# Kernel tuning notes

Measured on AMD Instinct MI355X. Metric: run time of the kernel, lower is better.

Reference implementation:

```python
import jax, jax.numpy as jnp
import numpy as np

SEQ_LEN = 1024
WINDOW = 32
NUM_HEADS = 16
BATCH = 8
DIM = 1024


def make_local_mask(seq_len=SEQ_LEN, window=WINDOW):
    # True = position is MASKED (disallowed), matching the torch bool attn_mask.
    # torch allows j in [i - window//2, i + window//2] inclusive.
    i = np.arange(seq_len)[:, None]
    j = np.arange(seq_len)[None, :]
    half = window // 2
    allowed = (j >= i - half) & (j <= i + half)
    return jnp.asarray(~allowed)


def setup_inputs() -> dict:
    key = jax.random.key(0)
    k_x, k_wi, k_wo = jax.random.split(key, 3)
    scale_in = 1.0 / np.sqrt(DIM)
    return {
        "x": jax.random.normal(k_x, (BATCH, SEQ_LEN, DIM), dtype=jnp.float32),
        "w_in": jax.random.normal(k_wi, (3 * DIM, DIM), dtype=jnp.float32) * scale_in,
        "b_in": jnp.zeros((3 * DIM,), dtype=jnp.float32),
        "w_out": jax.random.normal(k_wo, (DIM, DIM), dtype=jnp.float32) * scale_in,
        "b_out": jnp.zeros((DIM,), dtype=jnp.float32),
        "mask": make_local_mask(),
    }


def reference(x, w_in, b_in, w_out, b_out, mask):
    B, S, D = x.shape
    H = NUM_HEADS
    hd = D // H
    # fused in-projection (torch nn.MultiheadAttention self-attn path)
    qkv = x @ w_in.T + b_in                      # [B, S, 3D]
    q, k, v = jnp.split(qkv, 3, axis=-1)
    q = q.reshape(B, S, H, hd).transpose(0, 2, 1, 3)  # [B, H, S, hd]
    k = k.reshape(B, S, H, hd).transpose(0, 2, 1, 3)
    v = v.reshape(B, S, H, hd).transpose(0, 2, 1, 3)
    scores = jnp.einsum("bhqd,bhkd->bhqk", q, k) / jnp.sqrt(jnp.asarray(hd, x.dtype))
    neg = jnp.asarray(jnp.finfo(x.dtype).min, x.dtype)
    scores = jnp.where(mask[None, None, :, :], neg, scores)
    attn = jax.nn.softmax(scores, axis=-1)
    ctx = jnp.einsum("bhqk,bhkd->bhqd", attn, v)  # [B, H, S, hd]
    ctx = ctx.transpose(0, 2, 1, 3).reshape(B, S, D)
    return ctx @ w_out.T + b_out
```

## Files before the change

### kernel.cpp

```cpp
#include <hip/hip_runtime.h>

#define S_LEN   1024
#define NH      16
#define HD      64
#define BATCHN  8
#define DMODEL  1024
#define HALF_W  16

typedef __attribute__((ext_vector_type(8))) short bf16x8;
typedef __attribute__((ext_vector_type(4))) float f32x4;

__device__ __forceinline__ unsigned short f2bf(float f) {
  unsigned u = __builtin_bit_cast(unsigned, f);
  u += 0x7fffu + ((u >> 16) & 1u);
  return (unsigned short)(u >> 16);
}
__device__ __forceinline__ float bf2f(unsigned short h) {
  return __builtin_bit_cast(float, ((unsigned)h) << 16);
}

__device__ __forceinline__ void gload_lds16(const void* g, void* l) {
  __builtin_amdgcn_global_load_lds(
      (const __attribute__((address_space(1))) void*)g,
      (__attribute__((address_space(3))) void*)l, 16, 0, 0);
}

__global__ __launch_bounds__(256) void cvt_bf16_kernel(
    const float* __restrict__ in, unsigned short* __restrict__ out, int n4) {
  int t = blockIdx.x * 256 + threadIdx.x;
  if (t >= n4) return;
  float4 v = reinterpret_cast<const float4*>(in)[t];
  ushort4 o = make_ushort4(f2bf(v.x), f2bf(v.y), f2bf(v.z), f2bf(v.w));
  reinterpret_cast<ushort4*>(out)[t] = o;
}

#define MFMA_BF16 __builtin_amdgcn_mfma_f32_16x16x32_bf16

__global__ __launch_bounds__(512, 2) void gemm_inproj_kernel(
    const unsigned short* __restrict__ A,
    const unsigned short* __restrict__ B,
    const float* __restrict__ bias,
    unsigned short* __restrict__ C) {
  __shared__ __align__(16) unsigned short lds[81920];

  const int tid  = threadIdx.x;
  const int lane = tid & 63;
  const int wid  = tid >> 6;
  const int wm   = wid >> 2;
  const int wn   = wid & 3;
  const int lgrp = lane >> 4;
  const int l15  = lane & 15;

  const int sid = (blockIdx.x & 7) * 32 + (blockIdx.x >> 3);
  const int tileM = (sid >> 3) * 256;
  const int tileN = (sid & 7) * 384;

  const int srow = tid >> 2;
  const int scol = ((tid & 3) ^ ((tid >> 3) & 3)) * 8;
  const unsigned short* gA_s = A + (size_t)(tileM + srow) * 1024 + scol;
  const unsigned short* gB_s = B + (size_t)(tileN + srow) * 1024 + scol;

  const int fch  = (lgrp ^ ((l15 >> 1) & 3)) * 8;
  const int arow = (wm * 128 + l15) * 32 + fch;
  const int brow = (wn * 96 + l15) * 32 + fch;

  f32x4 acc[48] = {};

#define STG(S) do { const int _q = (S) & 3;                                \
    const unsigned short* _ga = gA_s + (S) * 32;                           \
    const unsigned short* _gb = gB_s + (S) * 32;                           \
    gload_lds16(_ga,          &lds[_q * 8192 + tid * 8]);                  \
    gload_lds16(_ga + 131072, &lds[_q * 8192 + 4096 + tid * 8]);           \
    gload_lds16(_gb,          &lds[32768 + _q * 12288 + tid * 8]);         \
    gload_lds16(_gb + 131072, &lds[32768 + _q * 12288 + 4096 + tid * 8]);  \
    gload_lds16(_gb + 262144, &lds[32768 + _q * 12288 + 8192 + tid * 8]);  \
  } while (0)

#define M24(MB)                                                            \
    acc[(MB+0)*6+0] = MFMA_BF16(a0_, b0_, acc[(MB+0)*6+0], 0, 0, 0);       \
    acc[(MB+0)*6+1] = MFMA_BF16(a0_, b1_, acc[(MB+0)*6+1], 0, 0, 0);       \
    acc[(MB+0)*6+2] = MFMA_BF16(a0_, b2_, acc[(MB+0)*6+2], 0, 0, 0);       \
    acc[(MB+0)*6+3] = MFMA_BF16(a0_, b3_, acc[(MB+0)*6+3], 0, 0, 0);       \
    acc[(MB+0)*6+4] = MFMA_BF16(a0_, b4_, acc[(MB+0)*6+4], 0, 0, 0);       \
    acc[(MB+0)*6+5] = MFMA_BF16(a0_, b5_, acc[(MB+0)*6+5], 0, 0, 0);       \
    acc[(MB+1)*6+0] = MFMA_BF16(a1_, b0_, acc[(MB+1)*6+0], 0, 0, 0);       \
    acc[(MB+1)*6+1] = MFMA_BF16(a1_, b1_, acc[(MB+1)*6+1], 0, 0, 0);       \
    acc[(MB+1)*6+2] = MFMA_BF16(a1_, b2_, acc[(MB+1)*6+2], 0, 0, 0);       \
    acc[(MB+1)*6+3] = MFMA_BF16(a1_, b3_, acc[(MB+1)*6+3], 0, 0, 0);       \
    acc[(MB+1)*6+4] = MFMA_BF16(a1_, b4_, acc[(MB+1)*6+4], 0, 0, 0);       \
    acc[(MB+1)*6+5] = MFMA_BF16(a1_, b5_, acc[(MB+1)*6+5], 0, 0, 0);       \
    acc[(MB+2)*6+0] = MFMA_BF16(a2_, b0_, acc[(MB+2)*6+0], 0, 0, 0);       \
    acc[(MB+2)*6+1] = MFMA_BF16(a2_, b1_, acc[(MB+2)*6+1], 0, 0, 0);       \
    acc[(MB+2)*6+2] = MFMA_BF16(a2_, b2_, acc[(MB+2)*6+2], 0, 0, 0);       \
    acc[(MB+2)*6+3] = MFMA_BF16(a2_, b3_, acc[(MB+2)*6+3], 0, 0, 0);       \
    acc[(MB+2)*6+4] = MFMA_BF16(a2_, b4_, acc[(MB+2)*6+4], 0, 0, 0);       \
    acc[(MB+2)*6+5] = MFMA_BF16(a2_, b5_, acc[(MB+2)*6+5], 0, 0, 0);       \
    acc[(MB+3)*6+0] = MFMA_BF16(a3_, b0_, acc[(MB+3)*6+0], 0, 0, 0);       \
    acc[(MB+3)*6+1] = MFMA_BF16(a3_, b1_, acc[(MB+3)*6+1], 0, 0, 0);       \
    acc[(MB+3)*6+2] = MFMA_BF16(a3_, b2_, acc[(MB+3)*6+2], 0, 0, 0);       \
    acc[(MB+3)*6+3] = MFMA_BF16(a3_, b3_, acc[(MB+3)*6+3], 0, 0, 0);       \
    acc[(MB+3)*6+4] = MFMA_BF16(a3_, b4_, acc[(MB+3)*6+4], 0, 0, 0);       \
    acc[(MB+3)*6+5] = MFMA_BF16(a3_, b5_, acc[(MB+3)*6+5], 0, 0, 0);

  STG(0); STG(1); STG(2);

#pragma unroll 1
  for (int p = 0; p < 32; ++p) {
    if (p < 30)       { asm volatile("s_waitcnt vmcnt(10)" ::: "memory"); }
    else if (p == 30) { asm volatile("s_waitcnt vmcnt(5)"  ::: "memory"); }
    else              { asm volatile("s_waitcnt vmcnt(0)"  ::: "memory"); }
    __builtin_amdgcn_sched_barrier(0);
    __builtin_amdgcn_s_barrier();

    if (p <= 28) STG(p + 3);

    const int slot = p & 3;
    const unsigned short* pa = &lds[slot * 8192 + arow];
    const unsigned short* pb = &lds[32768 + slot * 12288 + brow];

    bf16x8 b0_ = *(const bf16x8*)(pb);
    bf16x8 b1_ = *(const bf16x8*)(pb + 512);
    bf16x8 b2_ = *(const bf16x8*)(pb + 1024);
    bf16x8 b3_ = *(const bf16x8*)(pb + 1536);
    bf16x8 b4_ = *(const bf16x8*)(pb + 2048);
    bf16x8 b5_ = *(const bf16x8*)(pb + 2560);
    bf16x8 a0_ = *(const bf16x8*)(pa);
    bf16x8 a1_ = *(const bf16x8*)(pa + 512);
    bf16x8 a2_ = *(const bf16x8*)(pa + 1024);
    bf16x8 a3_ = *(const bf16x8*)(pa + 1536);
    asm volatile("s_waitcnt lgkmcnt(0)" ::: "memory");
    __builtin_amdgcn_sched_barrier(0);
    __builtin_amdgcn_s_setprio(1);
    M24(0)
    __builtin_amdgcn_s_setprio(0);

    a0_ = *(const bf16x8*)(pa + 2048);
    a1_ = *(const bf16x8*)(pa + 2560);
    a2_ = *(const bf16x8*)(pa + 3072);
    a3_ = *(const bf16x8*)(pa + 3584);
    asm volatile("s_waitcnt lgkmcnt(0)" ::: "memory");
    __builtin_amdgcn_sched_barrier(0);
    __builtin_amdgcn_s_setprio(1);
    M24(4)
    __builtin_amdgcn_s_setprio(0);
  }
#undef STG
#undef M24

#pragma unroll
  for (int nt = 0; nt < 6; ++nt) {
    const int col = tileN + wn * 96 + nt * 16 + l15;
    const float bs = bias[col];
#pragma unroll
    for (int mt = 0; mt < 8; ++mt) {
      const int row0 = tileM + wm * 128 + mt * 16 + lgrp * 4;
#pragma unroll
      for (int rr = 0; rr < 4; ++rr)
        C[(size_t)(row0 + rr) * 3072 + col] = f2bf(acc[mt * 6 + nt][rr] + bs);
    }
  }
}

__global__ __launch_bounds__(512, 2) void gemm_outproj_kernel(
    const unsigned short* __restrict__ A,
    const unsigned short* __restrict__ B,
    const float* __restrict__ bias,
    float* __restrict__ Cv) {
  __shared__ __align__(16) unsigned short sA[2][2][4096];
  __shared__ __align__(16) unsigned short sB[2][2][8192];

  const int tid  = threadIdx.x;
  const int lane = tid & 63;
  const int wid  = tid >> 6;
  const int wm   = wid >> 2;
  const int wn   = wid & 3;
  const int lgrp = lane >> 4;
  const int l15  = lane & 15;

  const int sid = (blockIdx.x & 7) * 32 + (blockIdx.x >> 3);
  const int tileM = (sid >> 2) * 128;
  const int tileN = (sid & 3) * 256;

  const int srow = tid >> 2;
  const int scol = ((tid & 3) ^ ((tid >> 3) & 3)) * 8;
  const unsigned short* gA_s = A + (size_t)(tileM + srow) * 1024 + scol;
  const unsigned short* gB_s = B + (size_t)(tileN + srow) * 1024 + scol;

  const int fch  = (lgrp ^ ((l15 >> 1) & 3)) * 8;
  const int arow = (wm * 64 + l15) * 32 + fch;
  const int brow = (wn * 64 + l15) * 32 + fch;

  f32x4 acc[4][4] = {};

#define SSA(KT, BUF, KH) do {                                              \
    gload_lds16(gA_s + (KT) * 64 + (KH) * 32, &sA[BUF][KH][wid * 512]);    \
  } while (0)
#define SSB(KT, BUF, KH) do {                                              \
    const unsigned short* _sb = gB_s + (KT) * 64 + (KH) * 32;              \
    gload_lds16(_sb,          &sB[BUF][KH][wid * 512]);                    \
    gload_lds16(_sb + 131072, &sB[BUF][KH][4096 + wid * 512]);             \
  } while (0)

#define GATE(NSTR) do {                                                    \
    asm volatile("s_waitcnt vmcnt(" NSTR ")" ::: "memory");                \
    __builtin_amdgcn_sched_barrier(0);                                     \
    __builtin_amdgcn_s_barrier(); } while (0)

#define PH1(BUF, KH, STGA, STGB) do {                                      \
    STGA; STGB;                                                            \
    const unsigned short* _pa = &sA[BUF][KH][arow];                        \
    const unsigned short* _pb = &sB[BUF][KH][brow];                        \
    bf16x8 a0_ = *(const bf16x8*)(_pa);                                    \
    bf16x8 a1_ = *(const bf16x8*)(_pa + 512);                              \
    bf16x8 a2_ = *(const bf16x8*)(_pa + 1024);                             \
    bf16x8 a3_ = *(const bf16x8*)(_pa + 1536);                             \
    bf16x8 nb0 = *(const bf16x8*)(_pb);                                    \
    bf16x8 nb1 = *(const bf16x8*)(_pb + 512);                              \
    bf16x8 nb2 = *(const bf16x8*)(_pb + 1024);                             \
    bf16x8 nb3 = *(const bf16x8*)(_pb + 1536);                             \
    asm volatile("s_waitcnt lgkmcnt(0)" ::: "memory");                     \
    __builtin_amdgcn_sched_barrier(0);                                     \
    __builtin_amdgcn_s_setprio(1);                                         \
    acc[0][0] = MFMA_BF16(a0_, nb0, acc[0][0], 0, 0, 0);                   \
    acc[0][1] = MFMA_BF16(a0_, nb1, acc[0][1], 0, 0, 0);                   \
    acc[0][2] = MFMA_BF16(a0_, nb2, acc[0][2], 0, 0, 0);                   \
    acc[0][3] = MFMA_BF16(a0_, nb3, acc[0][3], 0, 0, 0);                   \
    acc[1][0] = MFMA_BF16(a1_, nb0, acc[1][0], 0, 0, 0);                   \
    acc[1][1] = MFMA_BF16(a1_, nb1, acc[1][1], 0, 0, 0);                   \
    acc[1][2] = MFMA_BF16(a1_, nb2, acc[1][2], 0, 0, 0);                   \
    acc[1][3] = MFMA_BF16(a1_, nb3, acc[1][3], 0, 0, 0);                   \
    acc[2][0] = MFMA_BF16(a2_, nb0, acc[2][0], 0, 0, 0);                   \
    acc[2][1] = MFMA_BF16(a2_, nb1, acc[2][1], 0, 0, 0);                   \
    acc[2][2] = MFMA_BF16(a2_, nb2, acc[2][2], 0, 0, 0);                   \
    acc[2][3] = MFMA_BF16(a2_, nb3, acc[2][3], 0, 0, 0);                   \
    acc[3][0] = MFMA_BF16(a3_, nb0, acc[3][0], 0, 0, 0);                   \
    acc[3][1] = MFMA_BF16(a3_, nb1, acc[3][1], 0, 0, 0);                   \
    acc[3][2] = MFMA_BF16(a3_, nb2, acc[3][2], 0, 0, 0);                   \
    acc[3][3] = MFMA_BF16(a3_, nb3, acc[3][3], 0, 0, 0);                   \
    __builtin_amdgcn_s_setprio(0);                                         \
  } while (0)
#define NOSTG ((void)0)

  SSA(0, 0, 0); SSB(0, 0, 0);
  SSA(0, 0, 1); SSB(0, 0, 1);
  SSA(1, 1, 0); SSB(1, 1, 0);

#pragma unroll 1
  for (int kt = 0; kt < 14; kt += 2) {
    GATE("6"); PH1(0, 0, SSA(kt + 1, 1, 1), SSB(kt + 1, 1, 1));
    GATE("6"); PH1(0, 1, SSA(kt + 2, 0, 0), SSB(kt + 2, 0, 0));
    GATE("6"); PH1(1, 0, SSA(kt + 2, 0, 1), SSB(kt + 2, 0, 1));
    GATE("6"); PH1(1, 1, SSA(kt + 3, 1, 0), SSB(kt + 3, 1, 0));
  }
  GATE("6"); PH1(0, 0, SSA(15, 1, 1), SSB(15, 1, 1));
  GATE("6"); PH1(0, 1, NOSTG, NOSTG);
  GATE("3"); PH1(1, 0, NOSTG, NOSTG);
  GATE("0"); PH1(1, 1, NOSTG, NOSTG);

#undef SSA
#undef SSB
#undef GATE
#undef PH1
#undef NOSTG

#pragma unroll
  for (int nt = 0; nt < 4; ++nt) {
    const int col = tileN + wn * 64 + nt * 16 + l15;
    const float bs = bias[col];
#pragma unroll
    for (int mt = 0; mt < 4; ++mt) {
      const int row0 = tileM + wm * 64 + mt * 16 + lgrp * 4;
#pragma unroll
      for (int rr = 0; rr < 4; ++rr)
        Cv[(size_t)(row0 + rr) * 1024 + col] = acc[mt][nt][rr] + bs;
    }
  }
}

#define KST 72
#define PST 104

__global__ __launch_bounds__(256) void attn_local_kernel(
    const unsigned short* __restrict__ qkv, unsigned short* __restrict__ ctx) {
  __shared__ __align__(16) unsigned short sKP[96 * KST];
  __shared__ __align__(16) unsigned short sQ[64 * KST];
  __shared__ __align__(16) unsigned short sVT[64 * PST];

  const int tid  = threadIdx.x;
  const int lane = tid & 63;
  const int wid  = tid >> 6;
  const int qc   = lane & 15;
  const int lgrp = lane >> 4;

  const int qb = blockIdx.x & 15;
  const int h  = (blockIdx.x >> 4) & 15;
  const int b  = blockIdx.x >> 8;
  const int i0 = qb * 64;

  const unsigned short* hb = qkv + (size_t)b * S_LEN * 3072 + (size_t)h * HD;

#pragma unroll
  for (int it = 0; it < 3; ++it) {
    int c  = it * 256 + tid;
    int r  = c >> 3;
    int d0 = (c & 7) * 8;
    int j  = i0 - 16 + r;
    bf16x8 kv = {}, vv = {};
    if (0 <= j && j < S_LEN) {
      const unsigned short* rp = hb + (size_t)j * 3072;
      kv = *reinterpret_cast<const bf16x8*>(rp + DMODEL + d0);
      vv = *reinterpret_cast<const bf16x8*>(rp + 2 * DMODEL + d0);
    }
    *reinterpret_cast<bf16x8*>(&sKP[r * KST + d0]) = kv;
#pragma unroll
    for (int jj = 0; jj < 8; ++jj) {
      int dd = (jj + c) & 7;
      sVT[(d0 + dd) * PST + r] = (unsigned short)vv[dd];
    }
  }
#pragma unroll
  for (int it = 0; it < 2; ++it) {
    int c  = it * 256 + tid;
    int r  = c >> 3;
    int d0 = (c & 7) * 8;
    bf16x8 qv = *reinterpret_cast<const bf16x8*>(hb + (size_t)(i0 + r) * 3072 + d0);
    *reinterpret_cast<bf16x8*>(&sQ[r * KST + d0]) = qv;
  }
  __syncthreads();

  const int q0 = wid * 16;

  bf16x8 bq[2];
#pragma unroll
  for (int ks = 0; ks < 2; ++ks)
    bq[ks] = *reinterpret_cast<const bf16x8*>(
        &sQ[(q0 + qc) * KST + ks * 32 + lgrp * 8]);

  f32x4 st[6] = {};
#pragma unroll
  for (int kt = 0; kt < 6; ++kt) {
#pragma unroll
    for (int ks = 0; ks < 2; ++ks) {
      bf16x8 fa = *reinterpret_cast<const bf16x8*>(
          &sKP[(kt * 16 + qc) * KST + ks * 32 + lgrp * 8]);
      st[kt] = __builtin_amdgcn_mfma_f32_16x16x32_bf16(fa, bq[ks], st[kt], 0, 0, 0);
    }
  }
  __syncthreads();

  const int q = q0 + qc;
  float pv[6][4];
  float mx = -3.0e38f;
#pragma unroll
  for (int kt = 0; kt < 6; ++kt)
#pragma unroll
    for (int rr = 0; rr < 4; ++rr) {
      int kk = kt * 16 + lgrp * 4 + rr;
      int j  = i0 - 16 + kk;
      bool ok = (j >= 0) && (j < S_LEN) && (kk >= q) && (kk <= q + 32);
      float s = ok ? st[kt][rr] * 0.125f : -3.0e38f;
      pv[kt][rr] = s;
      mx = fmaxf(mx, s);
    }
  mx = fmaxf(mx, __shfl_xor(mx, 16, 64));
  mx = fmaxf(mx, __shfl_xor(mx, 32, 64));

  float rsum = 0.f;
#pragma unroll
  for (int kt = 0; kt < 6; ++kt)
#pragma unroll
    for (int rr = 0; rr < 4; ++rr) {
      float p = __expf(pv[kt][rr] - mx);
      pv[kt][rr] = p;
      rsum += p;
    }
  rsum += __shfl_xor(rsum, 16, 64);
  rsum += __shfl_xor(rsum, 32, 64);
  const float inv = 1.0f / rsum;

  unsigned short* sP = sKP;
#pragma unroll
  for (int kt = 0; kt < 6; ++kt) {
    ushort4 w = make_ushort4(f2bf(pv[kt][0]), f2bf(pv[kt][1]),
                             f2bf(pv[kt][2]), f2bf(pv[kt][3]));
    *reinterpret_cast<ushort4*>(&sP[(q0 + qc) * PST + kt * 16 + lgrp * 4]) = w;
  }

  bf16x8 pb[3];
#pragma unroll
  for (int ks = 0; ks < 3; ++ks)
    pb[ks] = *reinterpret_cast<const bf16x8*>(
        &sP[(q0 + qc) * PST + ks * 32 + lgrp * 8]);

  f32x4 ct[4] = {};
#pragma unroll
  for (int dt = 0; dt < 4; ++dt)
#pragma unroll
    for (int ks = 0; ks < 3; ++ks) {
      bf16x8 fa = *reinterpret_cast<const bf16x8*>(
          &sVT[(dt * 16 + qc) * PST + ks * 32 + lgrp * 8]);
      ct[dt] = __builtin_amdgcn_mfma_f32_16x16x32_bf16(fa, pb[ks], ct[dt], 0, 0, 0);
    }

  unsigned short* op =
      ctx + ((size_t)b * S_LEN + i0 + q0 + qc) * DMODEL + h * HD;
#pragma unroll
  for (int dt = 0; dt < 4; ++dt) {
    ushort4 w = make_ushort4(
        f2bf(ct[dt][0] * inv), f2bf(ct[dt][1] * inv),
        f2bf(ct[dt][2] * inv), f2bf(ct[dt][3] * inv));
    *reinterpret_cast<ushort4*>(op + dt * 16 + lgrp * 4) = w;
  }
}

extern "C" void kernel_launch(void* const* d_in, const int* in_sizes, int n_in,
                              void* d_out, int out_size, void* d_ws, size_t ws_size,
                              hipStream_t stream) {
  const float* x     = (const float*)d_in[0];
  const float* w_in  = (const float*)d_in[1];
  const float* b_in  = (const float*)d_in[2];
  const float* w_out = (const float*)d_in[3];
  const float* b_out = (const float*)d_in[4];
  float* out = (float*)d_out;

  unsigned short* xb   = (unsigned short*)d_ws;
  unsigned short* wib  = xb  + (size_t)8192 * 1024;
  unsigned short* wob  = wib + (size_t)3072 * 1024;
  unsigned short* qkv  = wob + (size_t)1024 * 1024;
  unsigned short* ctxb = qkv + (size_t)8192 * 3072;

  cvt_bf16_kernel<<<8192, 256, 0, stream>>>(x, xb, (8192 * 1024) / 4);
  cvt_bf16_kernel<<<3072, 256, 0, stream>>>(w_in, wib, (3072 * 1024) / 4);
  cvt_bf16_kernel<<<1024, 256, 0, stream>>>(w_out, wob, (1024 * 1024) / 4);

  gemm_inproj_kernel<<<256, 512, 0, stream>>>(xb, wib, b_in, qkv);

  attn_local_kernel<<<BATCHN * NH * (S_LEN / 64), 256, 0, stream>>>(qkv, ctxb);

  gemm_outproj_kernel<<<256, 512, 0, stream>>>(ctxb, wob, b_out, out);
}
```

Baseline: 121.2 us.

## Double-buffer LDS fragment registers to prefetch next k-step during MFMAs

Restructures the in-projection GEMM main loop into a ping-pong register scheme. The A/B fragments for the next k-slice are read from LDS while the current slice's MFMAs run, with partial lgkmcnt waits in place of full drains. The vmcnt waits are tightened to match the earlier fragment reads. This is meant to hide LDS read latency behind matrix work, at the cost of many more live VGPRs (about 24 extra bf16x8 registers) with occupancy fixed at 2 blocks of 512 threads, so spilling is a risk.

```diff
diff --git a/kernel.cpp b/kernel.cpp
--- a/kernel.cpp
+++ b/kernel.cpp
@@ -65,6 +65,12 @@
   const int brow = (wn * 96 + l15) * 32 + fch;
 
   f32x4 acc[48] = {};
+
+  bf16x8 b0A = {}, b1A = {}, b2A = {}, b3A = {}, b4A = {}, b5A = {};
+  bf16x8 a0A = {}, a1A = {}, a2A = {}, a3A = {};
+  bf16x8 b0B = {}, b1B = {}, b2B = {}, b3B = {}, b4B = {}, b5B = {};
+  bf16x8 a0B = {}, a1B = {}, a2B = {}, a3B = {};
+  bf16x8 sa0 = {}, sa1 = {}, sa2 = {}, sa3 = {};
 
 #define STG(S) do { const int _q = (S) & 3;                                \
     const unsigned short* _ga = gA_s + (S) * 32;                           \
@@ -76,76 +82,73 @@
     gload_lds16(_gb + 262144, &lds[32768 + _q * 12288 + 8192 + tid * 8]);  \
   } while (0)
 
-#define M24(MB)                                                            \
-    acc[(MB+0)*6+0] = MFMA_BF16(a0_, b0_, acc[(MB+0)*6+0], 0, 0, 0);       \
-    acc[(MB+0)*6+1] = MFMA_BF16(a0_, b1_, acc[(MB+0)*6+1], 0, 0, 0);       \
-    acc[(MB+0)*6+2] = MFMA_BF16(a0_, b2_, acc[(MB+0)*6+2], 0, 0, 0);       \
-    acc[(MB+0)*6+3] = MFMA_BF16(a0_, b3_, acc[(MB+0)*6+3], 0, 0, 0);       \
-    acc[(MB+0)*6+4] = MFMA_BF16(a0_, b4_, acc[(MB+0)*6+4], 0, 0, 0);       \
-    acc[(MB+0)*6+5] = MFMA_BF16(a0_, b5_, acc[(MB+0)*6+5], 0, 0, 0);       \
-    acc[(MB+1)*6+0] = MFMA_BF16(a1_, b0_, acc[(MB+1)*6+0], 0, 0, 0);       \
-    acc[(MB+1)*6+1] = MFMA_BF16(a1_, b1_, acc[(MB+1)*6+1], 0, 0, 0);       \
-    acc[(MB+1)*6+2] = MFMA_BF16(a1_, b2_, acc[(MB+1)*6+2], 0, 0, 0);       \
-    acc[(MB+1)*6+3] = MFMA_BF16(a1_, b3_, acc[(MB+1)*6+3], 0, 0, 0);       \
-    acc[(MB+1)*6+4] = MFMA_BF16(a1_, b4_, acc[(MB+1)*6+4], 0, 0, 0);       \
-    acc[(MB+1)*6+5] = MFMA_BF16(a1_, b5_, acc[(MB+1)*6+5], 0, 0, 0);       \
-    acc[(MB+2)*6+0] = MFMA_BF16(a2_, b0_, acc[(MB+2)*6+0], 0, 0, 0);       \
-    acc[(MB+2)*6+1] = MFMA_BF16(a2_, b1_, acc[(MB+2)*6+1], 0, 0, 0);       \
-    acc[(MB+2)*6+2] = MFMA_BF16(a2_, b2_, acc[(MB+2)*6+2], 0, 0, 0);       \
-    acc[(MB+2)*6+3] = MFMA_BF16(a2_, b3_, acc[(MB+2)*6+3], 0, 0, 0);       \
-    acc[(MB+2)*6+4] = MFMA_BF16(a2_, b4_, acc[(MB+2)*6+4], 0, 0, 0);       \
-    acc[(MB+2)*6+5] = MFMA_BF16(a2_, b5_, acc[(MB+2)*6+5], 0, 0, 0);       \
-    acc[(MB+3)*6+0] = MFMA_BF16(a3_, b0_, acc[(MB+3)*6+0], 0, 0, 0);       \
-    acc[(MB+3)*6+1] = MFMA_BF16(a3_, b1_, acc[(MB+3)*6+1], 0, 0, 0);       \
-    acc[(MB+3)*6+2] = MFMA_BF16(a3_, b2_, acc[(MB+3)*6+2], 0, 0, 0);       \
-    acc[(MB+3)*6+3] = MFMA_BF16(a3_, b3_, acc[(MB+3)*6+3], 0, 0, 0);       \
-    acc[(MB+3)*6+4] = MFMA_BF16(a3_, b4_, acc[(MB+3)*6+4], 0, 0, 0);       \
-    acc[(MB+3)*6+5] = MFMA_BF16(a3_, b5_, acc[(MB+3)*6+5], 0, 0, 0);
+#define ROW6(AV, MT, CU)                                                   \
+    acc[(MT)*6+0] = MFMA_BF16(AV, b0##CU, acc[(MT)*6+0], 0, 0, 0);         \
+    acc[(MT)*6+1] = MFMA_BF16(AV, b1##CU, acc[(MT)*6+1], 0, 0, 0);         \
+    acc[(MT)*6+2] = MFMA_BF16(AV, b2##CU, acc[(MT)*6+2], 0, 0, 0);         \
+    acc[(MT)*6+3] = MFMA_BF16(AV, b3##CU, acc[(MT)*6+3], 0, 0, 0);         \
+    acc[(MT)*6+4] = MFMA_BF16(AV, b4##CU, acc[(MT)*6+4], 0, 0, 0);         \
+    acc[(MT)*6+5] = MFMA_BF16(AV, b5##CU, acc[(MT)*6+5], 0, 0, 0);
+
+#define RD10(SET, SLOT) do {                                               \
+    const unsigned short* _pb = &lds[32768 + (SLOT) * 12288 + brow];       \
+    b0##SET = *(const bf16x8*)(_pb);                                       \
+    b1##SET = *(const bf16x8*)(_pb + 512);                                 \
+    b2##SET = *(const bf16x8*)(_pb + 1024);                                \
+    b3##SET = *(const bf16x8*)(_pb + 1536);                                \
+    b4##SET = *(const bf16x8*)(_pb + 2048);                                \
+    b5##SET = *(const bf16x8*)(_pb + 2560);                                \
+    const unsigned short* _pa = &lds[(SLOT) * 8192 + arow];                \
+    a0##SET = *(const bf16x8*)(_pa);                                       \
+    a1##SET = *(const bf16x8*)(_pa + 512);                                 \
+    a2##SET = *(const bf16x8*)(_pa + 1024);                                \
+    a3##SET = *(const bf16x8*)(_pa + 1536);                                \
+  } while (0)
+
+#define PH(P, CU, NX) do {                                                 \
+    if ((P) < 30) { asm volatile("s_waitcnt vmcnt(5)" ::: "memory"); }     \
+    else          { asm volatile("s_waitcnt vmcnt(0)" ::: "memory"); }     \
+    __builtin_amdgcn_sched_barrier(0);                                     \
+    __builtin_amdgcn_s_barrier();                                          \
+    if ((P) <= 28) STG((P) + 3);                                           \
+    { const unsigned short* _ps = &lds[((P) & 3) * 8192 + arow + 2048];    \
+      sa0 = *(const bf16x8*)(_ps);                                         \
+      sa1 = *(const bf16x8*)(_ps + 512);                                   \
+      sa2 = *(const bf16x8*)(_ps + 1024);                                  \
+      sa3 = *(const bf16x8*)(_ps + 1536); }                                \
+    if ((P) < 31) RD10(NX, ((P) + 1) & 3);                                 \
+    __builtin_amdgcn_sched_barrier(0);                                     \
+    if ((P) < 31) { asm volatile("s_waitcnt lgkmcnt(14)" ::: "memory"); }  \
+    else          { asm volatile("s_waitcnt lgkmcnt(4)"  ::: "memory"); }  \
+    __builtin_amdgcn_sched_barrier(0);                                     \
+    __builtin_amdgcn_s_setprio(1);                                         \
+    ROW6(a0##CU, 0, CU) ROW6(a1##CU, 1, CU)                                \
+    ROW6(a2##CU, 2, CU) ROW6(a3##CU, 3, CU)                                \
+    __builtin_amdgcn_s_setprio(0);                                         \
+    if ((P) < 31) { asm volatile("s_waitcnt lgkmcnt(10)" ::: "memory"); }  \
+    else          { asm volatile("s_waitcnt lgkmcnt(0)"  ::: "memory"); }  \
+    __builtin_amdgcn_sched_barrier(0);                                     \
+    __builtin_amdgcn_s_setprio(1);                                         \
+    ROW6(sa0, 4, CU) ROW6(sa1, 5, CU)                                      \
+    ROW6(sa2, 6, CU) ROW6(sa3, 7, CU)                                      \
+    __builtin_amdgcn_s_setprio(0);                                         \
+  } while (0)
 
   STG(0); STG(1); STG(2);
+  asm volatile("s_waitcnt vmcnt(10)" ::: "memory");
+  __builtin_amdgcn_sched_barrier(0);
+  __builtin_amdgcn_s_barrier();
+  RD10(A, 0);
 
 #pragma unroll 1
-  for (int p = 0; p < 32; ++p) {
-    if (p < 30)       { asm volatile("s_waitcnt vmcnt(10)" ::: "memory"); }
-    else if (p == 30) { asm volatile("s_waitcnt vmcnt(5)"  ::: "memory"); }
-    else              { asm volatile("s_waitcnt vmcnt(0)"  ::: "memory"); }
-    __builtin_amdgcn_sched_barrier(0);
-    __builtin_amdgcn_s_barrier();
-
-    if (p <= 28) STG(p + 3);
-
-    const int slot = p & 3;
-    const unsigned short* pa = &lds[slot * 8192 + arow];
-    const unsigned short* pb = &lds[32768 + slot * 12288 + brow];
-
-    bf16x8 b0_ = *(const bf16x8*)(pb);
-    bf16x8 b1_ = *(const bf16x8*)(pb + 512);
-    bf16x8 b2_ = *(const bf16x8*)(pb + 1024);
-    bf16x8 b3_ = *(const bf16x8*)(pb + 1536);
-    bf16x8 b4_ = *(const bf16x8*)(pb + 2048);
-    bf16x8 b5_ = *(const bf16x8*)(pb + 2560);
-    bf16x8 a0_ = *(const bf16x8*)(pa);
-    bf16x8 a1_ = *(const bf16x8*)(pa + 512);
-    bf16x8 a2_ = *(const bf16x8*)(pa + 1024);
-    bf16x8 a3_ = *(const bf16x8*)(pa + 1536);
-    asm volatile("s_waitcnt lgkmcnt(0)" ::: "memory");
-    __builtin_amdgcn_sched_barrier(0);
-    __builtin_amdgcn_s_setprio(1);
-    M24(0)
-    __builtin_amdgcn_s_setprio(0);
-
-    a0_ = *(const bf16x8*)(pa + 2048);
-    a1_ = *(const bf16x8*)(pa + 2560);
-    a2_ = *(const bf16x8*)(pa + 3072);
-    a3_ = *(const bf16x8*)(pa + 3584);
-    asm volatile("s_waitcnt lgkmcnt(0)" ::: "memory");
-    __builtin_amdgcn_sched_barrier(0);
-    __builtin_amdgcn_s_setprio(1);
-    M24(4)
-    __builtin_amdgcn_s_setprio(0);
+  for (int p = 0; p < 32; p += 2) {
+    PH(p, A, B);
+    PH(p + 1, B, A);
   }
 #undef STG
-#undef M24
+#undef ROW6
+#undef RD10
+#undef PH
 
 #pragma unroll
   for (int nt = 0; nt < 6; ++nt) {
```

Result: slower. 331.1 us (+173.1%).
